# Kernel tuning notes

Hardware: AMD Instinct MI355X
Metric: run time of the kernel (lower is better)

Reference implementation:

```python
import jax, jax.numpy as jnp
import numpy as np

B, S, E, H = 8, 1024, 512, 16
L = S            # block_len == seq_len (only valid operating point of the module)
D = E // H       # d_head = 32


def setup_inputs() -> dict:
    key = jax.random.key(0)
    k0, k1, k2, k3, k4 = jax.random.split(key, 5)
    scale = 1.0 / np.sqrt(E).astype(np.float32)
    return {
        "x": jax.random.normal(k0, (B, S, E), dtype=jnp.float32),
        "Wq": jax.random.normal(k1, (E, E), dtype=jnp.float32) * scale,  # torch Linear weight (out,in)
        "Wk": jax.random.normal(k2, (E, E), dtype=jnp.float32) * scale,
        "Wv": jax.random.normal(k3, (E, E), dtype=jnp.float32) * scale,
        "Er": jax.random.normal(k4, (2 * L - 1, D), dtype=jnp.float32),  # relative pos embeddings
    }


def reference(x, Wq, Wk, Wv, Er):
    b, s, e = x.shape
    l = s  # block_len == seq_len -> pad_len = 0, n_block = 1
    # projections (torch Linear: y = x @ W.T), split heads -> [b, h, l, d]
    q = (x @ Wq.T).reshape(b, s, H, D).transpose(0, 2, 1, 3)
    k = (x @ Wk.T).reshape(b, s, H, D).transpose(0, 2, 1, 3)
    v = (x @ Wv.T).reshape(b, s, H, D).transpose(0, 2, 1, 3)

    # content scores [b, h, l, l]
    QK = jnp.einsum('bhqd,bhkd->bhqk', q, k)

    # relative position bias. The pad/flatten/reshape skew trick in the original
    # is exactly Srel[i, j] = q[i] . Er[j - i + L - 1] (mask_QEr zeros entries
    # that the skew never reads). Implemented as a gather of Er + einsum.
    rel_idx = jnp.arange(l)[None, :] - jnp.arange(l)[:, None] + (l - 1)  # [l, l] in [0, 2l-2]
    Er_g = Er[rel_idx]                                                   # [l, l, d]
    Srel = jnp.einsum('bhid,ijd->bhij', q, Er_g)

    # NOTE: the module's causal `mask` buffer is never applied in forward.
    attn = jax.nn.softmax((QK + Srel) / np.sqrt(D).astype(np.float32), axis=-1)
    out = jnp.einsum('bhij,bhjd->bhid', attn, v)       # [b, h, l, d]
    out = out.transpose(0, 2, 1, 3).reshape(b, s, e)   # merge heads
    return out  # dropout is identity in eval / p=0
```

## Files before the change

kernel.cpp:

```cpp
#include <hip/hip_runtime.h>
#include <hip/hip_bf16.h>


typedef short bf16x8 __attribute__((ext_vector_type(8)));
typedef float f32x4 __attribute__((ext_vector_type(4)));
typedef unsigned short u16x4 __attribute__((ext_vector_type(4)));
typedef unsigned int u32x4 __attribute__((ext_vector_type(4)));

#if __has_builtin(__builtin_amdgcn_exp2f)
#define EXP2F(x) __builtin_amdgcn_exp2f(x)
#else
#define EXP2F(x) exp2f(x)
#endif

constexpr int Bb = 8, Ss = 1024, Ee = 512, Hh = 16, Dd = 32;
#define QSCALE 0.25503486f

__device__ __forceinline__ bf16x8 ldg_frag(const __hip_bfloat16* p) {
    return *reinterpret_cast<const bf16x8*>(p);
}

__device__ __forceinline__ unsigned short bf16_bits(float v) {
    return __builtin_bit_cast(unsigned short, __float2bfloat16(v));
}

__device__ __forceinline__ unsigned pack_bf16(float lo, float hi) {
    return (unsigned)bf16_bits(lo) | ((unsigned)bf16_bits(hi) << 16);
}

__device__ __forceinline__ float bperm_f(int addr, float v) {
    return __builtin_bit_cast(float,
        __builtin_amdgcn_ds_bpermute(addr, __builtin_bit_cast(int, v)));
}

__global__ __launch_bounds__(256) void convert_kernel(
    const float* __restrict__ x,  const float* __restrict__ wq,
    const float* __restrict__ wk, const float* __restrict__ wv,
    const float* __restrict__ er,
    __hip_bfloat16* __restrict__ xb, __hip_bfloat16* __restrict__ wb,
    __hip_bfloat16* __restrict__ erb)
{
    const int GX = 1048576, GW = 65536, GE = 16384;
    int g = blockIdx.x * 256 + threadIdx.x;
    const float* src;
    __hip_bfloat16* dst;
    int rel;
    if (g < GX)               { src = x;  dst = xb;          rel = g; }
    else if (g < GX +   GW)   { src = wq; dst = wb;          rel = g - GX; }
    else if (g < GX + 2*GW)   { src = wk; dst = wb + 262144; rel = g - GX - GW; }
    else if (g < GX + 3*GW)   { src = wv; dst = wb + 524288; rel = g - GX - 2*GW; }
    else                      { src = er; dst = erb;         rel = g - GX - 3*GW; }
    u16x4 pk = {0, 0, 0, 0};
    if (src != er || rel < 16376) {
        const float4 v = *reinterpret_cast<const float4*>(src + (size_t)rel * 4);
        pk[0] = bf16_bits(v.x);
        pk[1] = bf16_bits(v.y);
        pk[2] = bf16_bits(v.z);
        pk[3] = bf16_bits(v.w);
    }
    *reinterpret_cast<u16x4*>(dst + (size_t)rel * 4) = pk;
}

#define PROJ_LOAD(A, B, OFF) do {                                     \
    _Pragma("unroll")                                                 \
    for (int rf = 0; rf < 4; ++rf) A[rf] = ldg_frag(xp + rf * 16 * Ee + (OFF)); \
    _Pragma("unroll")                                                 \
    for (int t = 0; t < 4; ++t)    B[t] = ldg_frag(wp + t * 16 * Ee + (OFF)); \
} while (0)

#define PROJ_MFMA(A, B) do {                                          \
    _Pragma("unroll")                                                 \
    for (int rf = 0; rf < 4; ++rf)                                    \
        _Pragma("unroll")                                             \
        for (int t = 0; t < 4; ++t)                                   \
            acc[rf][t] = __builtin_amdgcn_mfma_f32_16x16x32_bf16(     \
                A[rf], B[t], acc[rf][t], 0, 0, 0);                    \
} while (0)

__global__ __launch_bounds__(256) void proj_kernel(
    const __hip_bfloat16* __restrict__ xb,
    const __hip_bfloat16* __restrict__ wb,
    __hip_bfloat16* __restrict__ Qs,
    __hip_bfloat16* __restrict__ Kh,
    unsigned* __restrict__ Vt32)
{
    const int tid  = threadIdx.x;
    const int wave = tid >> 6;
    const int lane = tid & 63;
    const int li   = lane & 15;
    const int quad = lane >> 4;

    const int by = blockIdx.x & 127;
    const int bx = blockIdx.x >> 7;
    const int m0    = by * 64;
    const int nbase = bx * 256 + wave * 64;
    const int mat   = nbase >> 9;
    const int nn0   = nbase & 511;

    f32x4 acc[4][4];
    #pragma unroll
    for (int rf = 0; rf < 4; ++rf)
        #pragma unroll
        for (int t = 0; t < 4; ++t) acc[rf][t] = f32x4{0.f, 0.f, 0.f, 0.f};

    const __hip_bfloat16* xp = xb + (size_t)(m0 + li) * Ee + quad * 8;
    const __hip_bfloat16* wp = wb + (size_t)(nbase + li) * Ee + quad * 8;

    bf16x8 aC[4], bC[4], aN[4], bN[4];
    PROJ_LOAD(aC, bC, 0);
    #pragma unroll
    for (int kk = 0; kk < 8; ++kk) {
        PROJ_LOAD(aN, bN, kk * 64 + 32);
        PROJ_MFMA(aC, bC);
        if (kk < 7) PROJ_LOAD(aC, bC, kk * 64 + 64);
        PROJ_MFMA(aN, bN);
    }

    const int bb = m0 >> 10;
    const int sb = m0 & 1023;
    if (mat == 2) {
        #pragma unroll
        for (int t = 0; t < 4; ++t) {
            int nn = nn0 + t * 16 + li;
            int h = nn >> 5, d = nn & 31;
            size_t base = ((size_t)(bb * Hh + h) * Dd + d) * 512
                        + (sb >> 5) * 16 + quad * 4;
            #pragma unroll
            for (int p = 0; p < 2; ++p) {
                u32x4 pk;
                #pragma unroll
                for (int r = 0; r < 4; ++r)
                    pk[r] = pack_bf16(acc[2*p][t][r], acc[2*p+1][t][r]);
                *reinterpret_cast<u32x4*>(Vt32 + base + (size_t)p * 16) = pk;
            }
        }
    } else {
        __hip_bfloat16* dst = (mat == 0) ? Qs : Kh;
        const float sc = (mat == 0) ? QSCALE : 1.0f;
        #pragma unroll
        for (int rf = 0; rf < 4; ++rf) {
            const int srow = sb + rf * 16 + quad * 4;
            #pragma unroll
            for (int t = 0; t < 4; ++t) {
                int nn = nn0 + t * 16 + li;
                int h = nn >> 5, d = nn & 31;
                #pragma unroll
                for (int r = 0; r < 4; ++r)
                    dst[((size_t)(bb * Hh + h) * Ss + (srow + r)) * Dd + d] =
                        __float2bfloat16(acc[rf][t][r] * sc);
            }
        }
    }
}

__global__ __launch_bounds__(256) void attn_kernel(
    const __hip_bfloat16* __restrict__ Qs,
    const __hip_bfloat16* __restrict__ Kh,
    const __hip_bfloat16* __restrict__ Vt,
    const __hip_bfloat16* __restrict__ Er,
    float* __restrict__ out)
{
    const int tid  = threadIdx.x;
    const int wave = tid >> 6;
    const int lane = tid & 63;
    const int li   = lane & 15;
    const int quad = lane >> 4;

    const int c  = blockIdx.x & 127;
    const int b  = c >> 4;
    const int h  = c & 15;
    const int ib = blockIdx.x >> 7;
    const int i0 = ib * 128 + wave * 32;

    const __hip_bfloat16* Qp = Qs + (size_t)(b * Hh + h) * Ss * Dd;
    const __hip_bfloat16* Kp = Kh + (size_t)(b * Hh + h) * Ss * Dd;
    const __hip_bfloat16* Vp = Vt + (size_t)(b * Hh + h) * Dd * Ss;

    __shared__ unsigned pb_lds[4][4][16 * 20];
    unsigned* pbA0 = pb_lds[wave][0];
    unsigned* pbA1 = pb_lds[wave][1];
    unsigned* pbB0 = pb_lds[wave][2];
    unsigned* pbB1 = pb_lds[wave][3];

    const bf16x8 qfA = ldg_frag(Qp + (i0      + li) * Dd + quad * 8);
    const bf16x8 qfB = ldg_frag(Qp + (i0 + 16 + li) * Dd + quad * 8);

    int addr4[4];
    bool cond[4];
    #pragma unroll
    for (int r = 0; r < 4; ++r) {
        const int row = quad * 4 + r;
        addr4[r] = (16 * quad + ((li - row + 15) & 15)) * 4;
        cond[r]  = (li <= row);
    }
    const int pbw = quad * 80 + li;
    const int pbr = li * 20 + quad * 4;

    f32x4 oA0 = f32x4{0,0,0,0}, oA1 = f32x4{0,0,0,0};
    f32x4 oB0 = f32x4{0,0,0,0}, oB1 = f32x4{0,0,0,0};
    float lsumA[4] = {0,0,0,0}, lsumB[4] = {0,0,0,0};
    const f32x4 zero = f32x4{0,0,0,0};

    for (int j0 = 0; j0 < Ss; j0 += 64) {
        bf16x8 k0 = ldg_frag(Kp + (j0      + li) * Dd + quad * 8);
        bf16x8 k1 = ldg_frag(Kp + (j0 + 16 + li) * Dd + quad * 8);
        bf16x8 k2 = ldg_frag(Kp + (j0 + 32 + li) * Dd + quad * 8);
        bf16x8 k3 = ldg_frag(Kp + (j0 + 48 + li) * Dd + quad * 8);
        const int rb = j0 - i0 + 1008;
        bf16x8 em = ldg_frag(Er + (rb - 16 + li) * Dd + quad * 8);
        bf16x8 e0 = ldg_frag(Er + (rb      + li) * Dd + quad * 8);
        bf16x8 e1 = ldg_frag(Er + (rb + 16 + li) * Dd + quad * 8);
        bf16x8 e2 = ldg_frag(Er + (rb + 32 + li) * Dd + quad * 8);
        bf16x8 e3 = ldg_frag(Er + (rb + 48 + li) * Dd + quad * 8);
        bf16x8 e4 = ldg_frag(Er + (rb + 64 + li) * Dd + quad * 8);
        bf16x8 v0 = ldg_frag(Vp + (li     ) * Ss + j0 + quad * 8);
        bf16x8 v1 = ldg_frag(Vp + (li + 16) * Ss + j0 + quad * 8);
        bf16x8 v2 = ldg_frag(Vp + (li     ) * Ss + j0 + 32 + quad * 8);
        bf16x8 v3 = ldg_frag(Vp + (li + 16) * Ss + j0 + 32 + quad * 8);

        {
            f32x4 s0 = __builtin_amdgcn_mfma_f32_16x16x32_bf16(qfA, k0, zero, 0, 0, 0);
            f32x4 s1 = __builtin_amdgcn_mfma_f32_16x16x32_bf16(qfA, k1, zero, 0, 0, 0);
            f32x4 s2 = __builtin_amdgcn_mfma_f32_16x16x32_bf16(qfA, k2, zero, 0, 0, 0);
            f32x4 s3 = __builtin_amdgcn_mfma_f32_16x16x32_bf16(qfA, k3, zero, 0, 0, 0);
            f32x4 q0 = __builtin_amdgcn_mfma_f32_16x16x32_bf16(qfA, e0, zero, 0, 0, 0);
            f32x4 q1 = __builtin_amdgcn_mfma_f32_16x16x32_bf16(qfA, e1, zero, 0, 0, 0);
            f32x4 q2 = __builtin_amdgcn_mfma_f32_16x16x32_bf16(qfA, e2, zero, 0, 0, 0);
            f32x4 q3 = __builtin_amdgcn_mfma_f32_16x16x32_bf16(qfA, e3, zero, 0, 0, 0);
            f32x4 q4 = __builtin_amdgcn_mfma_f32_16x16x32_bf16(qfA, e4, zero, 0, 0, 0);
            float p0[4], p1[4], p2[4], p3[4];
            #pragma unroll
            for (int r = 0; r < 4; ++r) {
                float f0 = bperm_f(addr4[r], q0[r]);
                float f1 = bperm_f(addr4[r], q1[r]);
                float f2 = bperm_f(addr4[r], q2[r]);
                float f3 = bperm_f(addr4[r], q3[r]);
                float f4 = bperm_f(addr4[r], q4[r]);
                p0[r] = EXP2F(s0[r] + (cond[r] ? f0 : f1));
                p1[r] = EXP2F(s1[r] + (cond[r] ? f1 : f2));
                p2[r] = EXP2F(s2[r] + (cond[r] ? f2 : f3));
                p3[r] = EXP2F(s3[r] + (cond[r] ? f3 : f4));
                lsumA[r] += (p0[r] + p1[r]) + (p2[r] + p3[r]);
            }
            #pragma unroll
            for (int r = 0; r < 4; ++r) {
                pbA0[pbw + 20 * r] = pack_bf16(p0[r], p1[r]);
                pbA1[pbw + 20 * r] = pack_bf16(p2[r], p3[r]);
            }
            bf16x8 pf0 = *reinterpret_cast<const bf16x8*>(&pbA0[pbr]);
            bf16x8 pf1 = *reinterpret_cast<const bf16x8*>(&pbA1[pbr]);
            oA0 = __builtin_amdgcn_mfma_f32_16x16x32_bf16(pf0, v0, oA0, 0, 0, 0);
            oA1 = __builtin_amdgcn_mfma_f32_16x16x32_bf16(pf0, v1, oA1, 0, 0, 0);
            oA0 = __builtin_amdgcn_mfma_f32_16x16x32_bf16(pf1, v2, oA0, 0, 0, 0);
            oA1 = __builtin_amdgcn_mfma_f32_16x16x32_bf16(pf1, v3, oA1, 0, 0, 0);
        }

        {
            f32x4 s0 = __builtin_amdgcn_mfma_f32_16x16x32_bf16(qfB, k0, zero, 0, 0, 0);
            f32x4 s1 = __builtin_amdgcn_mfma_f32_16x16x32_bf16(qfB, k1, zero, 0, 0, 0);
            f32x4 s2 = __builtin_amdgcn_mfma_f32_16x16x32_bf16(qfB, k2, zero, 0, 0, 0);
            f32x4 s3 = __builtin_amdgcn_mfma_f32_16x16x32_bf16(qfB, k3, zero, 0, 0, 0);
            f32x4 q0 = __builtin_amdgcn_mfma_f32_16x16x32_bf16(qfB, em, zero, 0, 0, 0);
            f32x4 q1 = __builtin_amdgcn_mfma_f32_16x16x32_bf16(qfB, e0, zero, 0, 0, 0);
            f32x4 q2 = __builtin_amdgcn_mfma_f32_16x16x32_bf16(qfB, e1, zero, 0, 0, 0);
            f32x4 q3 = __builtin_amdgcn_mfma_f32_16x16x32_bf16(qfB, e2, zero, 0, 0, 0);
            f32x4 q4 = __builtin_amdgcn_mfma_f32_16x16x32_bf16(qfB, e3, zero, 0, 0, 0);
            float p0[4], p1[4], p2[4], p3[4];
            #pragma unroll
            for (int r = 0; r < 4; ++r) {
                float f0 = bperm_f(addr4[r], q0[r]);
                float f1 = bperm_f(addr4[r], q1[r]);
                float f2 = bperm_f(addr4[r], q2[r]);
                float f3 = bperm_f(addr4[r], q3[r]);
                float f4 = bperm_f(addr4[r], q4[r]);
                p0[r] = EXP2F(s0[r] + (cond[r] ? f0 : f1));
                p1[r] = EXP2F(s1[r] + (cond[r] ? f1 : f2));
                p2[r] = EXP2F(s2[r] + (cond[r] ? f2 : f3));
                p3[r] = EXP2F(s3[r] + (cond[r] ? f3 : f4));
                lsumB[r] += (p0[r] + p1[r]) + (p2[r] + p3[r]);
            }
            #pragma unroll
            for (int r = 0; r < 4; ++r) {
                pbB0[pbw + 20 * r] = pack_bf16(p0[r], p1[r]);
                pbB1[pbw + 20 * r] = pack_bf16(p2[r], p3[r]);
            }
            bf16x8 pf0 = *reinterpret_cast<const bf16x8*>(&pbB0[pbr]);
            bf16x8 pf1 = *reinterpret_cast<const bf16x8*>(&pbB1[pbr]);
            oB0 = __builtin_amdgcn_mfma_f32_16x16x32_bf16(pf0, v0, oB0, 0, 0, 0);
            oB1 = __builtin_amdgcn_mfma_f32_16x16x32_bf16(pf0, v1, oB1, 0, 0, 0);
            oB0 = __builtin_amdgcn_mfma_f32_16x16x32_bf16(pf1, v2, oB0, 0, 0, 0);
            oB1 = __builtin_amdgcn_mfma_f32_16x16x32_bf16(pf1, v3, oB1, 0, 0, 0);
        }
    }

    #pragma unroll
    for (int r = 0; r < 4; ++r) {
        float va = lsumA[r], vb = lsumB[r];
        va += __shfl_xor(va, 1, 64);  vb += __shfl_xor(vb, 1, 64);
        va += __shfl_xor(va, 2, 64);  vb += __shfl_xor(vb, 2, 64);
        va += __shfl_xor(va, 4, 64);  vb += __shfl_xor(vb, 4, 64);
        va += __shfl_xor(va, 8, 64);  vb += __shfl_xor(vb, 8, 64);
        lsumA[r] = 1.0f / va;
        lsumB[r] = 1.0f / vb;
    }
    #pragma unroll
    for (int r = 0; r < 4; ++r) {
        const int srowA = i0 + quad * 4 + r;
        float* opA = out + ((size_t)b * Ss + srowA) * Ee + h * Dd;
        opA[li]      = oA0[r] * lsumA[r];
        opA[16 + li] = oA1[r] * lsumA[r];
        float* opB = opA + 16 * Ee;
        opB[li]      = oB0[r] * lsumB[r];
        opB[16 + li] = oB1[r] * lsumB[r];
    }
}

extern "C" void kernel_launch(void* const* d_in, const int* in_sizes, int n_in,
                              void* d_out, int out_size, void* d_ws, size_t ws_size,
                              hipStream_t stream) {
    const float* x  = (const float*)d_in[0];
    const float* Wq = (const float*)d_in[1];
    const float* Wk = (const float*)d_in[2];
    const float* Wv = (const float*)d_in[3];
    const float* Er = (const float*)d_in[4];
    float* out = (float*)d_out;

    __hip_bfloat16* xb  = reinterpret_cast<__hip_bfloat16*>(d_ws);
    __hip_bfloat16* wbb = xb  + (size_t)8192 * 512;
    __hip_bfloat16* erb = wbb + (size_t)1536 * 512;
    __hip_bfloat16* Qs  = erb + 65536;
    __hip_bfloat16* Kh  = Qs  + (size_t)Bb * Hh * Ss * Dd;
    __hip_bfloat16* Vt  = Kh  + (size_t)Bb * Hh * Ss * Dd;

    convert_kernel<<<4928, 256, 0, stream>>>(x, Wq, Wk, Wv, Er, xb, wbb, erb);
    proj_kernel<<<dim3(768), 256, 0, stream>>>(
        xb, wbb, Qs, Kh, reinterpret_cast<unsigned*>(Vt));
    attn_kernel<<<dim3(1024), 256, 0, stream>>>(Qs, Kh, Vt, erb, out);
}
```

Before: 195.3 us.

## Fuse fp32-to-bf16 conversion into projection and compute softmax row sums via MFMA

```diff
diff --git a/kernel.cpp b/kernel.cpp
--- a/kernel.cpp
+++ b/kernel.cpp
@@ -33,40 +33,16 @@
         __builtin_amdgcn_ds_bpermute(addr, __builtin_bit_cast(int, v)));
 }
 
-__global__ __launch_bounds__(256) void convert_kernel(
-    const float* __restrict__ x,  const float* __restrict__ wq,
-    const float* __restrict__ wk, const float* __restrict__ wv,
-    const float* __restrict__ er,
-    __hip_bfloat16* __restrict__ xb, __hip_bfloat16* __restrict__ wb,
-    __hip_bfloat16* __restrict__ erb)
-{
-    const int GX = 1048576, GW = 65536, GE = 16384;
-    int g = blockIdx.x * 256 + threadIdx.x;
-    const float* src;
-    __hip_bfloat16* dst;
-    int rel;
-    if (g < GX)               { src = x;  dst = xb;          rel = g; }
-    else if (g < GX +   GW)   { src = wq; dst = wb;          rel = g - GX; }
-    else if (g < GX + 2*GW)   { src = wk; dst = wb + 262144; rel = g - GX - GW; }
-    else if (g < GX + 3*GW)   { src = wv; dst = wb + 524288; rel = g - GX - 2*GW; }
-    else                      { src = er; dst = erb;         rel = g - GX - 3*GW; }
-    u16x4 pk = {0, 0, 0, 0};
-    if (src != er || rel < 16376) {
-        const float4 v = *reinterpret_cast<const float4*>(src + (size_t)rel * 4);
-        pk[0] = bf16_bits(v.x);
-        pk[1] = bf16_bits(v.y);
-        pk[2] = bf16_bits(v.z);
-        pk[3] = bf16_bits(v.w);
-    }
-    *reinterpret_cast<u16x4*>(dst + (size_t)rel * 4) = pk;
-}
-
-#define PROJ_LOAD(A, B, OFF) do {                                     \
-    _Pragma("unroll")                                                 \
-    for (int rf = 0; rf < 4; ++rf) A[rf] = ldg_frag(xp + rf * 16 * Ee + (OFF)); \
-    _Pragma("unroll")                                                 \
-    for (int t = 0; t < 4; ++t)    B[t] = ldg_frag(wp + t * 16 * Ee + (OFF)); \
-} while (0)
+__device__ __forceinline__ bf16x8 ldg_f32_frag(const float* p) {
+    const float4 a = *reinterpret_cast<const float4*>(p);
+    const float4 b = *reinterpret_cast<const float4*>(p + 4);
+    u32x4 pk;
+    pk[0] = pack_bf16(a.x, a.y);
+    pk[1] = pack_bf16(a.z, a.w);
+    pk[2] = pack_bf16(b.x, b.y);
+    pk[3] = pack_bf16(b.z, b.w);
+    return __builtin_bit_cast(bf16x8, pk);
+}
 
 #define PROJ_MFMA(A, B) do {                                          \
     _Pragma("unroll")                                                 \
@@ -78,13 +54,33 @@
 } while (0)
 
 __global__ __launch_bounds__(256) void proj_kernel(
-    const __hip_bfloat16* __restrict__ xb,
-    const __hip_bfloat16* __restrict__ wb,
-    __hip_bfloat16* __restrict__ Qs,
-    __hip_bfloat16* __restrict__ Kh,
-    unsigned* __restrict__ Vt32)
+    const float* __restrict__ x,
+    const float* __restrict__ wq,
+    const float* __restrict__ wk,
+    const float* __restrict__ wv,
+    const float* __restrict__ er,
+    unsigned* __restrict__ Qs32,
+    unsigned* __restrict__ Kh32,
+    unsigned* __restrict__ Vt32,
+    unsigned* __restrict__ erb32)
 {
-    const int tid  = threadIdx.x;
+    const int tid = threadIdx.x;
+
+    if (blockIdx.x >= 768) {
+        const int id2 = (blockIdx.x - 768) * 256 + tid;
+        #pragma unroll
+        for (int p = 0; p < 2; ++p) {
+            const int s   = id2 * 2 + p;
+            const int row = s >> 4;
+            const int j   = s & 15;
+            unsigned val = 0;
+            if (row < 2047)
+                val = pack_bf16(er[row * 32 + j], er[row * 32 + j + 16]);
+            erb32[s] = val;
+        }
+        return;
+    }
+
     const int wave = tid >> 6;
     const int lane = tid & 63;
     const int li   = lane & 15;
@@ -96,6 +92,7 @@
     const int nbase = bx * 256 + wave * 64;
     const int mat   = nbase >> 9;
     const int nn0   = nbase & 511;
+    const float* W  = (mat == 0) ? wq : (mat == 1) ? wk : wv;
 
     f32x4 acc[4][4];
     #pragma unroll
@@ -103,17 +100,16 @@
         #pragma unroll
         for (int t = 0; t < 4; ++t) acc[rf][t] = f32x4{0.f, 0.f, 0.f, 0.f};
 
-    const __hip_bfloat16* xp = xb + (size_t)(m0 + li) * Ee + quad * 8;
-    const __hip_bfloat16* wp = wb + (size_t)(nbase + li) * Ee + quad * 8;
-
-    bf16x8 aC[4], bC[4], aN[4], bN[4];
-    PROJ_LOAD(aC, bC, 0);
-    #pragma unroll
-    for (int kk = 0; kk < 8; ++kk) {
-        PROJ_LOAD(aN, bN, kk * 64 + 32);
-        PROJ_MFMA(aC, bC);
-        if (kk < 7) PROJ_LOAD(aC, bC, kk * 64 + 64);
-        PROJ_MFMA(aN, bN);
+    const float* xp = x + (size_t)(m0 + li) * Ee + quad * 8;
+    const float* wp = W + (size_t)(nn0 + li) * Ee + quad * 8;
+
+    for (int k0 = 0; k0 < Ee; k0 += 32) {
+        bf16x8 a[4], b[4];
+        #pragma unroll
+        for (int rf = 0; rf < 4; ++rf) a[rf] = ldg_f32_frag(xp + rf * 16 * Ee + k0);
+        #pragma unroll
+        for (int t = 0; t < 4; ++t)    b[t]  = ldg_f32_frag(wp + t * 16 * Ee + k0);
+        PROJ_MFMA(a, b);
     }
 
     const int bb = m0 >> 10;
@@ -135,19 +131,18 @@
             }
         }
     } else {
-        __hip_bfloat16* dst = (mat == 0) ? Qs : Kh;
+        unsigned* dst = (mat == 0) ? Qs32 : Kh32;
         const float sc = (mat == 0) ? QSCALE : 1.0f;
+        const int h0 = nn0 >> 5;
         #pragma unroll
         for (int rf = 0; rf < 4; ++rf) {
-            const int srow = sb + rf * 16 + quad * 4;
-            #pragma unroll
-            for (int t = 0; t < 4; ++t) {
-                int nn = nn0 + t * 16 + li;
-                int h = nn >> 5, d = nn & 31;
+            #pragma unroll
+            for (int r = 0; r < 4; ++r) {
+                const int srow = sb + rf * 16 + quad * 4 + r;
                 #pragma unroll
-                for (int r = 0; r < 4; ++r)
-                    dst[((size_t)(bb * Hh + h) * Ss + (srow + r)) * Dd + d] =
-                        __float2bfloat16(acc[rf][t][r] * sc);
+                for (int hp = 0; hp < 2; ++hp)
+                    dst[((size_t)(bb * Hh + h0 + hp) * Ss + srow) * 16 + li] =
+                        pack_bf16(acc[rf][2*hp][r] * sc, acc[rf][2*hp+1][r] * sc);
             }
         }
     }
@@ -196,10 +191,10 @@
     const int pbw = quad * 80 + li;
     const int pbr = li * 20 + quad * 4;
 
-    f32x4 oA0 = f32x4{0,0,0,0}, oA1 = f32x4{0,0,0,0};
-    f32x4 oB0 = f32x4{0,0,0,0}, oB1 = f32x4{0,0,0,0};
-    float lsumA[4] = {0,0,0,0}, lsumB[4] = {0,0,0,0};
+    const bf16x8 onesb = {16256,16256,16256,16256,16256,16256,16256,16256};
     const f32x4 zero = f32x4{0,0,0,0};
+    f32x4 oA0 = zero, oA1 = zero, oB0 = zero, oB1 = zero;
+    f32x4 oLA = zero, oLB = zero;
 
     for (int j0 = 0; j0 < Ss; j0 += 64) {
         bf16x8 k0 = ldg_frag(Kp + (j0      + li) * Dd + quad * 8);
@@ -240,7 +235,6 @@
                 p1[r] = EXP2F(s1[r] + (cond[r] ? f1 : f2));
                 p2[r] = EXP2F(s2[r] + (cond[r] ? f2 : f3));
                 p3[r] = EXP2F(s3[r] + (cond[r] ? f3 : f4));
-                lsumA[r] += (p0[r] + p1[r]) + (p2[r] + p3[r]);
             }
             #pragma unroll
             for (int r = 0; r < 4; ++r) {
@@ -251,8 +245,10 @@
             bf16x8 pf1 = *reinterpret_cast<const bf16x8*>(&pbA1[pbr]);
             oA0 = __builtin_amdgcn_mfma_f32_16x16x32_bf16(pf0, v0, oA0, 0, 0, 0);
             oA1 = __builtin_amdgcn_mfma_f32_16x16x32_bf16(pf0, v1, oA1, 0, 0, 0);
+            oLA = __builtin_amdgcn_mfma_f32_16x16x32_bf16(pf0, onesb, oLA, 0, 0, 0);
             oA0 = __builtin_amdgcn_mfma_f32_16x16x32_bf16(pf1, v2, oA0, 0, 0, 0);
             oA1 = __builtin_amdgcn_mfma_f32_16x16x32_bf16(pf1, v3, oA1, 0, 0, 0);
+            oLA = __builtin_amdgcn_mfma_f32_16x16x32_bf16(pf1, onesb, oLA, 0, 0, 0);
         }
 
         {
@@ -277,7 +273,6 @@
                 p1[r] = EXP2F(s1[r] + (cond[r] ? f1 : f2));
                 p2[r] = EXP2F(s2[r] + (cond[r] ? f2 : f3));
                 p3[r] = EXP2F(s3[r] + (cond[r] ? f3 : f4));
-                lsumB[r] += (p0[r] + p1[r]) + (p2[r] + p3[r]);
             }
             #pragma unroll
             for (int r = 0; r < 4; ++r) {
@@ -288,30 +283,24 @@
             bf16x8 pf1 = *reinterpret_cast<const bf16x8*>(&pbB1[pbr]);
             oB0 = __builtin_amdgcn_mfma_f32_16x16x32_bf16(pf0, v0, oB0, 0, 0, 0);
             oB1 = __builtin_amdgcn_mfma_f32_16x16x32_bf16(pf0, v1, oB1, 0, 0, 0);
+            oLB = __builtin_amdgcn_mfma_f32_16x16x32_bf16(pf0, onesb, oLB, 0, 0, 0);
             oB0 = __builtin_amdgcn_mfma_f32_16x16x32_bf16(pf1, v2, oB0, 0, 0, 0);
             oB1 = __builtin_amdgcn_mfma_f32_16x16x32_bf16(pf1, v3, oB1, 0, 0, 0);
+            oLB = __builtin_amdgcn_mfma_f32_16x16x32_bf16(pf1, onesb, oLB, 0, 0, 0);
         }
     }
 
     #pragma unroll
     for (int r = 0; r < 4; ++r) {
-        float va = lsumA[r], vb = lsumB[r];
-        va += __shfl_xor(va, 1, 64);  vb += __shfl_xor(vb, 1, 64);
-        va += __shfl_xor(va, 2, 64);  vb += __shfl_xor(vb, 2, 64);
-        va += __shfl_xor(va, 4, 64);  vb += __shfl_xor(vb, 4, 64);
-        va += __shfl_xor(va, 8, 64);  vb += __shfl_xor(vb, 8, 64);
-        lsumA[r] = 1.0f / va;
-        lsumB[r] = 1.0f / vb;
-    }
-    #pragma unroll
-    for (int r = 0; r < 4; ++r) {
+        const float ia  = 1.0f / oLA[r];
+        const float ib2 = 1.0f / oLB[r];
         const int srowA = i0 + quad * 4 + r;
         float* opA = out + ((size_t)b * Ss + srowA) * Ee + h * Dd;
-        opA[li]      = oA0[r] * lsumA[r];
-        opA[16 + li] = oA1[r] * lsumA[r];
+        opA[li]      = oA0[r] * ia;
+        opA[16 + li] = oA1[r] * ia;
         float* opB = opA + 16 * Ee;
-        opB[li]      = oB0[r] * lsumB[r];
-        opB[16 + li] = oB1[r] * lsumB[r];
+        opB[li]      = oB0[r] * ib2;
+        opB[16 + li] = oB1[r] * ib2;
     }
 }
 
@@ -325,15 +314,14 @@
     const float* Er = (const float*)d_in[4];
     float* out = (float*)d_out;
 
-    __hip_bfloat16* xb  = reinterpret_cast<__hip_bfloat16*>(d_ws);
-    __hip_bfloat16* wbb = xb  + (size_t)8192 * 512;
-    __hip_bfloat16* erb = wbb + (size_t)1536 * 512;
+    __hip_bfloat16* erb = reinterpret_cast<__hip_bfloat16*>(d_ws);
     __hip_bfloat16* Qs  = erb + 65536;
     __hip_bfloat16* Kh  = Qs  + (size_t)Bb * Hh * Ss * Dd;
     __hip_bfloat16* Vt  = Kh  + (size_t)Bb * Hh * Ss * Dd;
 
-    convert_kernel<<<4928, 256, 0, stream>>>(x, Wq, Wk, Wv, Er, xb, wbb, erb);
-    proj_kernel<<<dim3(768), 256, 0, stream>>>(
-        xb, wbb, Qs, Kh, reinterpret_cast<unsigned*>(Vt));
+    proj_kernel<<<dim3(832), 256, 0, stream>>>(
+        x, Wq, Wk, Wv, Er,
+        reinterpret_cast<unsigned*>(Qs), reinterpret_cast<unsigned*>(Kh),
+        reinterpret_cast<unsigned*>(Vt), reinterpret_cast<unsigned*>(erb));
     attn_kernel<<<dim3(1024), 256, 0, stream>>>(Qs, Kh, Vt, erb, out);
 }
```

Result: slower. 227.5 us (+16.5%).
